# Kernel tuning notes

Measured on AMD Instinct MI355X. Metric: run time of the kernel, lower is better.

The kernel has to match this reference:

```python
import jax, jax.numpy as jnp
import numpy as np

N_NODES = 50000
N_EDGES = 800000
IN_F = 96
OUT_F = 128
K = 4


def setup_inputs() -> dict:
    key = jax.random.key(0)
    k1, k2, k3, k4, k5, k6 = jax.random.split(key, 6)
    x = jax.random.normal(k1, (N_NODES, IN_F), dtype=jnp.float32)
    lap_rows = jax.random.randint(k2, (N_EDGES,), 0, N_NODES, dtype=jnp.int32)
    lap_cols = jax.random.randint(k3, (N_EDGES,), 0, N_NODES, dtype=jnp.int32)
    # scaled-Laplacian-like values (small so the recurrence stays bounded)
    lap_vals = jax.random.normal(k4, (N_EDGES,), dtype=jnp.float32) * (1.0 / 16.0)
    # nn.Linear(in_features*k, out_features) params
    bound = 1.0 / np.sqrt(IN_F * K)
    W = jax.random.uniform(k5, (OUT_F, IN_F * K), dtype=jnp.float32, minval=-bound, maxval=bound)
    b = jax.random.uniform(k6, (OUT_F,), dtype=jnp.float32, minval=-bound, maxval=bound)
    return {"x": x, "lap_rows": lap_rows, "lap_cols": lap_cols, "lap_vals": lap_vals, "W": W, "b": b}


def reference(x, lap_rows, lap_cols, lap_vals, W, b):
    n = x.shape[0]

    def spmm(v):
        # y[r] = sum_{e: row[e]==r} vals[e] * v[col[e]]  -- sparse L @ v
        return jax.ops.segment_sum(lap_vals[:, None] * v[lap_cols], lap_rows, num_segments=n)

    # Chebyshev recurrence: T0 = x, T1 = L x, T_k = 2 L T_{k-1} - T_{k-2}
    xs = [x]
    x0 = x
    x1 = spmm(x0)
    xs.append(x1)
    for _ in range(2, K):
        x2 = 2.0 * spmm(x1) - x0
        xs.append(x2)
        x0, x1 = x1, x2
    # torch cat on dim=2 then view(N,-1): K is the fastest-varying axis
    cheb = jnp.stack(xs, axis=2).reshape(n, IN_F * K)  # [N, F*K]
    return cheb @ W.T + b
```

## Files before the change

kernel.cpp:

```cpp
#include <hip/hip_runtime.h>

#define N_NODES 50000
#define N_PAD 50048
#define N_EDGES 800000
#define IN_F 96
#define NDW 48
#define OUT_F 128
#define KTOT 384

#define NB 782
#define EPB 4096
#define NBLK ((N_EDGES + EPB - 1) / EPB)

#define SPMM_BLOCKS 4096

typedef __attribute__((ext_vector_type(8))) short bf16x8;
typedef __attribute__((ext_vector_type(4))) float f32x4;

__device__ __forceinline__ short f2bf(float x) {
  union { float f; unsigned u; } c;
  c.f = x;
  unsigned u = c.u;
  u = (u + 0x7FFFu + ((u >> 16) & 1u)) >> 16;
  return (short)u;
}

__device__ __forceinline__ float bflo(unsigned u) {
  union { unsigned u; float f; } c;
  c.u = u << 16;
  return c.f;
}
__device__ __forceinline__ float bfhi(unsigned u) {
  union { unsigned u; float f; } c;
  c.u = u & 0xffff0000u;
  return c.f;
}


__global__ __launch_bounds__(256) void passA_kernel(const int* __restrict__ rows,
                                                    int* __restrict__ hist) {
  __shared__ int h[NB];
  int B = blockIdx.x;
  for (int b = threadIdx.x; b < NB; b += 256) h[b] = 0;
  __syncthreads();
  int end = min((B + 1) * EPB, N_EDGES);
  for (int i = B * EPB + threadIdx.x; i < end; i += 256) atomicAdd(&h[rows[i] >> 6], 1);
  __syncthreads();
  for (int b = threadIdx.x; b < NB; b += 256) hist[b * NBLK + B] = h[b];
}

__global__ __launch_bounds__(256) void scanA_kernel(const int* __restrict__ hist,
                                                    int* __restrict__ off,
                                                    int* __restrict__ total) {
  __shared__ int tmp[256];
  int b = blockIdx.x;
  int tid = threadIdx.x;
  int v = (tid < NBLK) ? hist[b * NBLK + tid] : 0;
  tmp[tid] = v;
  __syncthreads();
  for (int o = 1; o < 256; o <<= 1) {
    int t = (tid >= o) ? tmp[tid - o] : 0;
    __syncthreads();
    tmp[tid] += t;
    __syncthreads();
  }
  if (tid < NBLK) off[b * NBLK + tid] = tmp[tid] - v;
  if (tid == 255) total[b] = tmp[tid];
}

__global__ __launch_bounds__(1024) void scanB_kernel(const int* __restrict__ total,
                                                     int* __restrict__ bucket_start) {
  __shared__ int tmp[1024];
  int tid = threadIdx.x;
  int v = (tid < NB) ? total[tid] : 0;
  tmp[tid] = v;
  __syncthreads();
  for (int o = 1; o < 1024; o <<= 1) {
    int t = (tid >= o) ? tmp[tid - o] : 0;
    __syncthreads();
    tmp[tid] += t;
    __syncthreads();
  }
  if (tid < NB) bucket_start[tid] = tmp[tid] - v;
  if (tid == 0) bucket_start[NB] = N_EDGES;
}

__global__ __launch_bounds__(256) void passB_kernel(
    const int* __restrict__ rows, const int* __restrict__ cols,
    const float* __restrict__ vals, const int* __restrict__ off,
    const int* __restrict__ bucket_start, int2* __restrict__ recs) {
  __shared__ int cur[NB];
  int B = blockIdx.x;
  for (int b = threadIdx.x; b < NB; b += 256)
    cur[b] = bucket_start[b] + off[b * NBLK + B];
  __syncthreads();
  int end = min((B + 1) * EPB, N_EDGES);
  for (int i = B * EPB + threadIdx.x; i < end; i += 256) {
    int r = rows[i];
    int pos = atomicAdd(&cur[r >> 6], 1);
    recs[pos] = make_int2((cols[i] & 0xffff) | ((r & 63) << 16), __float_as_int(vals[i]));
  }
}

__global__ __launch_bounds__(256) void bsort_kernel(
    const int* __restrict__ bucket_start, const int2* __restrict__ recs,
    int2* __restrict__ recs2, int* __restrict__ row_start) {
  __shared__ int hist[64], excl[64], cur[64];
  int b = blockIdx.x;
  int tid = threadIdx.x;
  if (tid < 64) hist[tid] = 0;
  __syncthreads();
  int s = bucket_start[b], e = bucket_start[b + 1];
  for (int i = s + tid; i < e; i += 256) atomicAdd(&hist[(recs[i].x >> 16) & 63], 1);
  __syncthreads();
  if (tid == 0) {
    int acc = 0;
    for (int j = 0; j < 64; ++j) {
      excl[j] = acc;
      acc += hist[j];
    }
  }
  __syncthreads();
  if (tid < 64) {
    cur[tid] = excl[tid];
    int r = b * 64 + tid;
    if (r < N_NODES) row_start[r] = s + excl[tid];
  }
  if (b == 0 && tid == 0) row_start[N_NODES] = N_EDGES;
  __syncthreads();
  for (int i = s + tid; i < e; i += 256) {
    int2 rec = recs[i];
    int lr = (rec.x >> 16) & 63;
    int pos = s + atomicAdd(&cur[lr], 1);
    recs2[pos] = make_int2(rec.x & 0xffff, rec.y);
  }
}


#define NXD (N_NODES * NDW)

__global__ void convert_xw_kernel(const float* __restrict__ x, unsigned* __restrict__ xb,
                                  const float* __restrict__ W, short* __restrict__ Wb) {
  int i = blockIdx.x * blockDim.x + threadIdx.x;
  if (i < NXD) {
    float2 v = reinterpret_cast<const float2*>(x)[i];
    xb[i] = (unsigned)(unsigned short)f2bf(v.x) | ((unsigned)(unsigned short)f2bf(v.y) << 16);
  } else if (i < NXD + OUT_F * KTOT) {
    int j = i - NXD;
    int o = j / KTOT;
    int r = j - o * KTOT;
    int k = r / IN_F;
    int f = r - k * IN_F;
    Wb[j] = f2bf(W[o * KTOT + f * 4 + k]);
  }
}


__global__ __launch_bounds__(256) void spmm_cheb_kernel(
    const int* __restrict__ row_start, const int2* __restrict__ recs,
    const short* __restrict__ vb,
    const short* __restrict__ prevb,
    float alpha, float beta,
    unsigned* __restrict__ yb) {
  int wid = blockIdx.x * 4 + (threadIdx.x >> 6);
  int lane = threadIdx.x & 63;
  int eslot = lane >> 3;
  int lid = lane & 7;
  const int stride = SPMM_BLOCKS * 4;

  for (int row = wid; row < N_NODES; row += stride) {
    int s = row_start[row];
    int e = row_start[row + 1];

    float acc[12];
#pragma unroll
    for (int i = 0; i < 12; ++i) acc[i] = 0.f;

    int idx = s + eslot;
    int2 rec = (idx < e) ? recs[idx] : make_int2(0, 0);

    for (int base = s; base < e; base += 8) {
      int2 cur = rec;
      int nidx = base + 8 + eslot;
      rec = (nidx < e) ? recs[nidx] : make_int2(0, 0);
      int c = cur.x;
      float val = __int_as_float(cur.y);
      const uint2* srcq = reinterpret_cast<const uint2*>(vb + (size_t)c * IN_F);
      uint2 q0 = srcq[lid];
      uint2 q1 = srcq[8 + lid];
      uint2 q2 = srcq[16 + lid];
      acc[0] += val * bflo(q0.x);
      acc[1] += val * bfhi(q0.x);
      acc[2] += val * bflo(q0.y);
      acc[3] += val * bfhi(q0.y);
      acc[4] += val * bflo(q1.x);
      acc[5] += val * bfhi(q1.x);
      acc[6] += val * bflo(q1.y);
      acc[7] += val * bfhi(q1.y);
      acc[8] += val * bflo(q2.x);
      acc[9] += val * bfhi(q2.x);
      acc[10] += val * bflo(q2.y);
      acc[11] += val * bfhi(q2.y);
    }

#pragma unroll
    for (int i = 0; i < 12; ++i) {
      acc[i] += __shfl_xor(acc[i], 8);
      acc[i] += __shfl_xor(acc[i], 16);
      acc[i] += __shfl_xor(acc[i], 32);
    }

    if (eslot < 6) {
      int it = eslot >> 1, j = eslot & 1;
      int d = it * 16 + 2 * lid + j;
      unsigned pv = reinterpret_cast<const unsigned*>(prevb + (size_t)row * IN_F)[d];
      float r0 = alpha * acc[4 * it + 2 * j] + beta * bflo(pv);
      float r1 = alpha * acc[4 * it + 2 * j + 1] + beta * bfhi(pv);
      yb[(size_t)row * NDW + d] =
          (unsigned)(unsigned short)f2bf(r0) | ((unsigned)(unsigned short)f2bf(r1) << 16);
    }
  }
}


__global__ __launch_bounds__(256) void gemm_mfma_kernel(
    const short* __restrict__ s0, const short* __restrict__ s1,
    const short* __restrict__ s2, const short* __restrict__ s3,
    const short* __restrict__ Bm,
    const float* __restrict__ bias,
    float* __restrict__ out) {
  int tid = threadIdx.x;
  int wave = tid >> 6;
  int lane = tid & 63;
  int n0 = blockIdx.x * 64;
  int o0 = wave * 32;
  int lr = lane & 15;
  int lk = (lane >> 4) * 8;

  f32x4 acc[4][2];
#pragma unroll
  for (int m = 0; m < 4; ++m)
#pragma unroll
    for (int nn = 0; nn < 2; ++nn) acc[m][nn] = (f32x4){0.f, 0.f, 0.f, 0.f};

  const short* segs[4] = {s0, s1, s2, s3};
  const short* bptr = Bm + (size_t)(o0 + lr) * KTOT + lk;

#pragma unroll
  for (int seg = 0; seg < 4; ++seg) {
    const short* aseg = segs[seg] + (size_t)(n0 + lr) * IN_F + lk;
#pragma unroll
    for (int t = 0; t < 3; ++t) {
      int kt = seg * 3 + t;
      bf16x8 a[4], b[2];
#pragma unroll
      for (int m = 0; m < 4; ++m)
        a[m] = *reinterpret_cast<const bf16x8*>(aseg + (size_t)m * 16 * IN_F + t * 32);
#pragma unroll
      for (int nn = 0; nn < 2; ++nn)
        b[nn] = *reinterpret_cast<const bf16x8*>(bptr + (size_t)nn * 16 * KTOT + kt * 32);
#pragma unroll
      for (int m = 0; m < 4; ++m)
#pragma unroll
        for (int nn = 0; nn < 2; ++nn)
          acc[m][nn] = __builtin_amdgcn_mfma_f32_16x16x32_bf16(a[m], b[nn], acc[m][nn], 0, 0, 0);
    }
  }

  int orow = (lane >> 4) * 4;
#pragma unroll
  for (int m = 0; m < 4; ++m) {
#pragma unroll
    for (int nn = 0; nn < 2; ++nn) {
      int oc = o0 + nn * 16 + lr;
      float bv = bias[oc];
#pragma unroll
      for (int j = 0; j < 4; ++j) {
        int n = n0 + m * 16 + orow + j;
        if (n < N_NODES) out[(size_t)n * OUT_F + oc] = acc[m][nn][j] + bv;
      }
    }
  }
}


extern "C" void kernel_launch(void* const* d_in, const int* in_sizes, int n_in,
                              void* d_out, int out_size, void* d_ws, size_t ws_size,
                              hipStream_t stream) {
  const float* x = (const float*)d_in[0];
  const int* lap_rows = (const int*)d_in[1];
  const int* lap_cols = (const int*)d_in[2];
  const float* lap_vals = (const float*)d_in[3];
  const float* W = (const float*)d_in[4];
  const float* b = (const float*)d_in[5];
  float* out = (float*)d_out;

  char* ws = (char*)d_ws;
  short* xb = (short*)ws;            ws += (size_t)N_NODES * IN_F * 2;
  short* T1b = (short*)ws;           ws += (size_t)N_NODES * IN_F * 2;
  short* T2b = (short*)ws;           ws += (size_t)N_NODES * IN_F * 2;
  short* T3b = (short*)ws;           ws += (size_t)N_NODES * IN_F * 2;
  short* Wb = (short*)ws;            ws += (size_t)OUT_F * KTOT * 2;
  int* hist = (int*)ws;              ws += (size_t)NB * NBLK * 4;
  int* off = (int*)ws;               ws += (size_t)NB * NBLK * 4;
  int* total = (int*)ws;             ws += (size_t)NB * 4;
  int* bucket_start = (int*)ws;      ws += (size_t)(NB + 2) * 4;
  int* row_start = (int*)ws;         ws += (size_t)(N_NODES + 8) * 4;
  ws = (char*)(((size_t)ws + 15) & ~(size_t)15);
  int2* recs = (int2*)ws;            ws += (size_t)N_EDGES * 8;
  int2* recs2 = (int2*)ws;           ws += (size_t)N_EDGES * 8;

  passA_kernel<<<NBLK, 256, 0, stream>>>(lap_rows, hist);
  scanA_kernel<<<NB, 256, 0, stream>>>(hist, off, total);
  scanB_kernel<<<1, 1024, 0, stream>>>(total, bucket_start);
  passB_kernel<<<NBLK, 256, 0, stream>>>(lap_rows, lap_cols, lap_vals, off, bucket_start,
                                         recs);
  bsort_kernel<<<NB, 256, 0, stream>>>(bucket_start, recs, recs2, row_start);

  convert_xw_kernel<<<(NXD + OUT_F * KTOT + 255) / 256, 256, 0, stream>>>(x, (unsigned*)xb,
                                                                          W, Wb);

  spmm_cheb_kernel<<<SPMM_BLOCKS, 256, 0, stream>>>(row_start, recs2, xb, xb, 1.f, 0.f,
                                                    (unsigned*)T1b);
  spmm_cheb_kernel<<<SPMM_BLOCKS, 256, 0, stream>>>(row_start, recs2, T1b, xb, 2.f, -1.f,
                                                    (unsigned*)T2b);
  spmm_cheb_kernel<<<SPMM_BLOCKS, 256, 0, stream>>>(row_start, recs2, T2b, T1b, 2.f, -1.f,
                                                    (unsigned*)T3b);

  gemm_mfma_kernel<<<N_PAD / 64, 256, 0, stream>>>(xb, T1b, T2b, T3b, Wb, b, out);
}
```

Before: 231.2 us.

## Split feature dimension into 32-wide slices to shrink SpMM gather working set

After: 298.5 us. 1.29x slower.

```diff
diff --git a/kernel.cpp b/kernel.cpp
--- a/kernel.cpp
+++ b/kernel.cpp
@@ -4,7 +4,6 @@
 #define N_PAD 50048
 #define N_EDGES 800000
 #define IN_F 96
-#define NDW 48
 #define OUT_F 128
 #define KTOT 384
 
@@ -13,6 +12,9 @@
 #define NBLK ((N_EDGES + EPB - 1) / EPB)
 
 #define SPMM_BLOCKS 4096
+
+#define PSTR ((size_t)N_PAD * 32)
+#define PQ ((size_t)N_PAD * 8)
 
 typedef __attribute__((ext_vector_type(8))) short bf16x8;
 typedef __attribute__((ext_vector_type(4))) float f32x4;
@@ -137,14 +139,19 @@
 }
 
 
-#define NXD (N_NODES * NDW)
+#define NXD (N_NODES * 48)
 
 __global__ void convert_xw_kernel(const float* __restrict__ x, unsigned* __restrict__ xb,
                                   const float* __restrict__ W, short* __restrict__ Wb) {
   int i = blockIdx.x * blockDim.x + threadIdx.x;
   if (i < NXD) {
     float2 v = reinterpret_cast<const float2*>(x)[i];
-    xb[i] = (unsigned)(unsigned short)f2bf(v.x) | ((unsigned)(unsigned short)f2bf(v.y) << 16);
+    int n = i / 48;
+    int d = i - n * 48;
+    int p = d >> 4;
+    int pd = d & 15;
+    xb[p * (N_PAD * 16) + n * 16 + pd] =
+        (unsigned)(unsigned short)f2bf(v.x) | ((unsigned)(unsigned short)f2bf(v.y) << 16);
   } else if (i < NXD + OUT_F * KTOT) {
     int j = i - NXD;
     int o = j / KTOT;
@@ -156,12 +163,12 @@
 }
 
 
-__global__ __launch_bounds__(256) void spmm_cheb_kernel(
+__global__ __launch_bounds__(256) void spmm_slice_kernel(
     const int* __restrict__ row_start, const int2* __restrict__ recs,
-    const short* __restrict__ vb,
-    const short* __restrict__ prevb,
+    const uint2* __restrict__ vq,
+    const uint2* __restrict__ pq,
     float alpha, float beta,
-    unsigned* __restrict__ yb) {
+    uint2* __restrict__ yq) {
   int wid = blockIdx.x * 4 + (threadIdx.x >> 6);
   int lane = threadIdx.x & 63;
   int eslot = lane >> 3;
@@ -172,52 +179,54 @@
     int s = row_start[row];
     int e = row_start[row + 1];
 
-    float acc[12];
-#pragma unroll
-    for (int i = 0; i < 12; ++i) acc[i] = 0.f;
+    uint2 pv = make_uint2(0u, 0u);
+    if (eslot == 0) pv = pq[(size_t)row * 8 + lid];
+
+    float acc[4] = {0.f, 0.f, 0.f, 0.f};
 
     int idx = s + eslot;
-    int2 rec = (idx < e) ? recs[idx] : make_int2(0, 0);
-
-    for (int base = s; base < e; base += 8) {
-      int2 cur = rec;
+    int2 rec0 = (idx < e) ? recs[idx] : make_int2(0, 0);
+    uint2 g0 = vq[(size_t)rec0.x * 8 + lid];
+
+    int base = s;
+    for (; base + 8 < e; base += 8) {
       int nidx = base + 8 + eslot;
-      rec = (nidx < e) ? recs[nidx] : make_int2(0, 0);
-      int c = cur.x;
-      float val = __int_as_float(cur.y);
-      const uint2* srcq = reinterpret_cast<const uint2*>(vb + (size_t)c * IN_F);
-      uint2 q0 = srcq[lid];
-      uint2 q1 = srcq[8 + lid];
-      uint2 q2 = srcq[16 + lid];
-      acc[0] += val * bflo(q0.x);
-      acc[1] += val * bfhi(q0.x);
-      acc[2] += val * bflo(q0.y);
-      acc[3] += val * bfhi(q0.y);
-      acc[4] += val * bflo(q1.x);
-      acc[5] += val * bfhi(q1.x);
-      acc[6] += val * bflo(q1.y);
-      acc[7] += val * bfhi(q1.y);
-      acc[8] += val * bflo(q2.x);
-      acc[9] += val * bfhi(q2.x);
-      acc[10] += val * bflo(q2.y);
-      acc[11] += val * bfhi(q2.y);
-    }
-
-#pragma unroll
-    for (int i = 0; i < 12; ++i) {
+      int2 rec1 = (nidx < e) ? recs[nidx] : make_int2(0, 0);
+      uint2 g1 = vq[(size_t)rec1.x * 8 + lid];
+
+      float val = __int_as_float(rec0.y);
+      acc[0] += val * bflo(g0.x);
+      acc[1] += val * bfhi(g0.x);
+      acc[2] += val * bflo(g0.y);
+      acc[3] += val * bfhi(g0.y);
+
+      rec0 = rec1;
+      g0 = g1;
+    }
+    {
+      float val = __int_as_float(rec0.y);
+      acc[0] += val * bflo(g0.x);
+      acc[1] += val * bfhi(g0.x);
+      acc[2] += val * bflo(g0.y);
+      acc[3] += val * bfhi(g0.y);
+    }
+
+#pragma unroll
+    for (int i = 0; i < 4; ++i) {
       acc[i] += __shfl_xor(acc[i], 8);
       acc[i] += __shfl_xor(acc[i], 16);
       acc[i] += __shfl_xor(acc[i], 32);
     }
 
-    if (eslot < 6) {
-      int it = eslot >> 1, j = eslot & 1;
-      int d = it * 16 + 2 * lid + j;
-      unsigned pv = reinterpret_cast<const unsigned*>(prevb + (size_t)row * IN_F)[d];
-      float r0 = alpha * acc[4 * it + 2 * j] + beta * bflo(pv);
-      float r1 = alpha * acc[4 * it + 2 * j + 1] + beta * bfhi(pv);
-      yb[(size_t)row * NDW + d] =
-          (unsigned)(unsigned short)f2bf(r0) | ((unsigned)(unsigned short)f2bf(r1) << 16);
+    if (eslot == 0) {
+      float r0 = alpha * acc[0] + beta * bflo(pv.x);
+      float r1 = alpha * acc[1] + beta * bfhi(pv.x);
+      float r2 = alpha * acc[2] + beta * bflo(pv.y);
+      float r3 = alpha * acc[3] + beta * bfhi(pv.y);
+      uint2 o;
+      o.x = (unsigned)(unsigned short)f2bf(r0) | ((unsigned)(unsigned short)f2bf(r1) << 16);
+      o.y = (unsigned)(unsigned short)f2bf(r2) | ((unsigned)(unsigned short)f2bf(r3) << 16);
+      yq[(size_t)row * 8 + lid] = o;
     }
   }
 }
@@ -248,14 +257,14 @@
 
 #pragma unroll
   for (int seg = 0; seg < 4; ++seg) {
-    const short* aseg = segs[seg] + (size_t)(n0 + lr) * IN_F + lk;
 #pragma unroll
     for (int t = 0; t < 3; ++t) {
       int kt = seg * 3 + t;
+      const short* aseg = segs[seg] + (size_t)t * PSTR + (size_t)(n0 + lr) * 32 + lk;
       bf16x8 a[4], b[2];
 #pragma unroll
       for (int m = 0; m < 4; ++m)
-        a[m] = *reinterpret_cast<const bf16x8*>(aseg + (size_t)m * 16 * IN_F + t * 32);
+        a[m] = *reinterpret_cast<const bf16x8*>(aseg + (size_t)m * 16 * 32);
 #pragma unroll
       for (int nn = 0; nn < 2; ++nn)
         b[nn] = *reinterpret_cast<const bf16x8*>(bptr + (size_t)nn * 16 * KTOT + kt * 32);
@@ -296,10 +305,10 @@
   float* out = (float*)d_out;
 
   char* ws = (char*)d_ws;
-  short* xb = (short*)ws;            ws += (size_t)N_NODES * IN_F * 2;
-  short* T1b = (short*)ws;           ws += (size_t)N_NODES * IN_F * 2;
-  short* T2b = (short*)ws;           ws += (size_t)N_NODES * IN_F * 2;
-  short* T3b = (short*)ws;           ws += (size_t)N_NODES * IN_F * 2;
+  short* xb = (short*)ws;            ws += (size_t)N_PAD * IN_F * 2;
+  short* T1b = (short*)ws;           ws += (size_t)N_PAD * IN_F * 2;
+  short* T2b = (short*)ws;           ws += (size_t)N_PAD * IN_F * 2;
+  short* T3b = (short*)ws;           ws += (size_t)N_PAD * IN_F * 2;
   short* Wb = (short*)ws;            ws += (size_t)OUT_F * KTOT * 2;
   int* hist = (int*)ws;              ws += (size_t)NB * NBLK * 4;
   int* off = (int*)ws;               ws += (size_t)NB * NBLK * 4;
@@ -320,12 +329,18 @@
   convert_xw_kernel<<<(NXD + OUT_F * KTOT + 255) / 256, 256, 0, stream>>>(x, (unsigned*)xb,
                                                                           W, Wb);
 
-  spmm_cheb_kernel<<<SPMM_BLOCKS, 256, 0, stream>>>(row_start, recs2, xb, xb, 1.f, 0.f,
-                                                    (unsigned*)T1b);
-  spmm_cheb_kernel<<<SPMM_BLOCKS, 256, 0, stream>>>(row_start, recs2, T1b, xb, 2.f, -1.f,
-                                                    (unsigned*)T2b);
-  spmm_cheb_kernel<<<SPMM_BLOCKS, 256, 0, stream>>>(row_start, recs2, T2b, T1b, 2.f, -1.f,
-                                                    (unsigned*)T3b);
+  uint2* xq = (uint2*)xb;
+  uint2* t1q = (uint2*)T1b;
+  uint2* t2q = (uint2*)T2b;
+  uint2* t3q = (uint2*)T3b;
+  for (int s = 0; s < 3; ++s) {
+    spmm_slice_kernel<<<SPMM_BLOCKS, 256, 0, stream>>>(row_start, recs2, xq + s * PQ,
+                                                       xq + s * PQ, 1.f, 0.f, t1q + s * PQ);
+    spmm_slice_kernel<<<SPMM_BLOCKS, 256, 0, stream>>>(row_start, recs2, t1q + s * PQ,
+                                                       xq + s * PQ, 2.f, -1.f, t2q + s * PQ);
+    spmm_slice_kernel<<<SPMM_BLOCKS, 256, 0, stream>>>(row_start, recs2, t2q + s * PQ,
+                                                       t1q + s * PQ, 2.f, -1.f, t3q + s * PQ);
+  }
 
   gemm_mfma_kernel<<<N_PAD / 64, 256, 0, stream>>>(xb, T1b, T2b, T3b, Wb, b, out);
 }
```
